# Optimization experiments

Measured on AMD Instinct MI355X. Metric: run time of the kernel, lower is better.

Reference implementation:

```python
import jax, jax.numpy as jnp
import numpy as np

DIM = 384
HEADS = 6
HEAD_DIM = DIM // HEADS
SCALE = HEAD_DIM ** -0.5


def setup_inputs() -> dict:
    key = jax.random.key(0)
    k1, k2, k3, k4, k5 = jax.random.split(key, 5)
    B, N, C = 2, 4096, DIM
    x = jax.random.normal(k1, (B, N, C), dtype=jnp.float32)
    mask = jax.random.randint(k2, (B, N), 0, 2) > 0  # bool [B, N]
    w_qkv = jax.random.normal(k3, (3 * C, C), dtype=jnp.float32) * (C ** -0.5)
    w_proj = jax.random.normal(k4, (C, C), dtype=jnp.float32) * (C ** -0.5)
    b_proj = jax.random.normal(k5, (C,), dtype=jnp.float32) * 0.01
    return {"x": x, "mask": mask, "w_qkv": w_qkv, "w_proj": w_proj, "b_proj": b_proj}


def reference(x, mask, w_qkv, w_proj, b_proj):
    B, N, C = x.shape
    # qkv projection (no bias), split into q, k, v of shape [B, H, N, hd]
    qkv = (x @ w_qkv.T).reshape(B, N, 3, HEADS, HEAD_DIM).transpose(2, 0, 3, 1, 4)
    q, k, v = qkv[0], qkv[1], qkv[2]
    attn = jnp.einsum('bhqd,bhkd->bhqk', q, k) * SCALE  # [B, H, N, N]
    # pairwise mask: mask[:, None, :] * mask[:, :, None], broadcast over heads
    pair = (mask[:, None, :, None] & mask[:, None, None, :])  # [B, 1, N, N]
    neg = -jnp.finfo(attn.dtype).max
    attn = jnp.where(pair, attn, neg)
    attn = jax.nn.softmax(attn, axis=-1)
    out = jnp.einsum('bhqk,bhkd->bhqd', attn, v)  # [B, H, N, hd]
    out = out.transpose(0, 2, 1, 3).reshape(B, N, C)
    return out @ w_proj.T + b_proj
```

## Files before the change

kernel.cpp:

```cpp
#include <hip/hip_runtime.h>
#include <cfloat>
#include <cstdint>
#include <cstddef>

using u16 = unsigned short;
typedef __attribute__((ext_vector_type(8))) short short8;
typedef __attribute__((ext_vector_type(4))) float f32x4;

#define HEADS 6
#define NSEQ 4096
#define SCALEF 0.125f
#define LOG2E 1.4426950408889634f
#define SC2 (SCALEF * LOG2E)

#if __has_builtin(__builtin_amdgcn_exp2f)
#define EXP2(x) __builtin_amdgcn_exp2f(x)
#else
#define EXP2(x) exp2f(x)
#endif

__device__ __forceinline__ u16 f2bf_rn(float f) {
  unsigned int u = __builtin_bit_cast(unsigned int, f);
  u = (u + 0x7FFFu + ((u >> 16) & 1u)) >> 16;
  return (u16)u;
}

__device__ __forceinline__ void gload_lds16(const void* g, void* l) {
  __builtin_amdgcn_global_load_lds((const __attribute__((address_space(1))) void*)g,
                                   (__attribute__((address_space(3))) void*)l, 16, 0, 0);
}

__device__ __forceinline__ short8 frag_read(const u16* tile, int row, int blk) {
  int byt = row * 128 + ((blk * 16) ^ ((row & 7) << 4));
  return *(const short8*)((const char*)tile + byt);
}

__device__ __forceinline__ void cast8(const float* __restrict__ s, u16* __restrict__ d, int i) {
  const float4* sp = (const float4*)s;
  float4 a = sp[2 * i], b = sp[2 * i + 1];
  short8 r;
  r[0] = (short)f2bf_rn(a.x); r[1] = (short)f2bf_rn(a.y);
  r[2] = (short)f2bf_rn(a.z); r[3] = (short)f2bf_rn(a.w);
  r[4] = (short)f2bf_rn(b.x); r[5] = (short)f2bf_rn(b.y);
  r[6] = (short)f2bf_rn(b.z); r[7] = (short)f2bf_rn(b.w);
  ((short8*)d)[i] = r;
}

__global__ void prep_kernel(const float* __restrict__ x, const float* __restrict__ wqkv,
                            const float* __restrict__ wproj, const int* __restrict__ mask,
                            u16* __restrict__ xb, u16* __restrict__ wqb, u16* __restrict__ wpb,
                            float* __restrict__ madd) {
  const int NX = 3145728 / 8, NQ = 442368 / 8, NP = 147456 / 8;
  int i = blockIdx.x * blockDim.x + threadIdx.x;
  if (i < NX) cast8(x, xb, i);
  else if (i < NX + NQ) cast8(wqkv, wqb, i - NX);
  else if (i < NX + NQ + NP) cast8(wproj, wpb, i - NX - NQ);
  else {
    int j = i - (NX + NQ + NP);
    if (j < 2 * NSEQ) madd[j] = mask[j] ? 0.f : -FLT_MAX;
  }
}

__global__ void compact_kernel(const int* __restrict__ mask, int* __restrict__ cpos,
                               float* __restrict__ acm, int* __restrict__ nth) {
  __shared__ int cnt[256];
  __shared__ int offu[256];
  __shared__ int s_nc;
  int b = blockIdx.x;
  int t = threadIdx.x;
  const int* m = mask + b * NSEQ;
  int base = t * 16;
  int c = 0;
#pragma unroll
  for (int i = 0; i < 16; ++i) c += (m[base + i] != 0) ? 1 : 0;
  cnt[t] = c;
  __syncthreads();
  if (t == 0) {
    int s = 0;
    for (int i = 0; i < 256; ++i) { offu[i] = s; s += cnt[i]; }
    s_nc = s;
    int ncpad = (s + 127) & ~127;
    if (ncpad == 0) ncpad = 128;
    nth[b] = ncpad / 128;
  }
  __syncthreads();
  int nc = s_nc;
  int ou = offu[t];
  int om = base - ou;
  for (int i = 0; i < 16; ++i) {
    int n = base + i;
    int um = (m[n] != 0) ? 1 : 0;
    int pos = um ? ou : (nc + om);
    ou += um;
    om += 1 - um;
    cpos[b * NSEQ + n] = pos;
    acm[b * NSEQ + pos] = um ? 0.f : -FLT_MAX;
  }
}

__global__ void meanv_kernel(const u16* __restrict__ vt, float* __restrict__ meanv) {
  int row = blockIdx.x;
  const u16* src = vt + (size_t)row * NSEQ + threadIdx.x * 8;
  float s = 0.f;
#pragma unroll
  for (int i = 0; i < 8; ++i) {
    short8 v = *(const short8*)(src + i * 512);
#pragma unroll
    for (int j = 0; j < 8; ++j) {
      unsigned int u = ((unsigned int)(unsigned short)v[j]) << 16;
      s += __builtin_bit_cast(float, u);
    }
  }
#pragma unroll
  for (int off = 1; off < 64; off <<= 1) s += __shfl_xor(s, off);
  if (threadIdx.x == 0) meanv[row] = s * (1.0f / NSEQ);
}

template <int EPI>
__launch_bounds__(256)
__global__ void gemm_bt(const u16* __restrict__ A, const u16* __restrict__ B,
                        int Kdim, int Ndim,
                        u16* __restrict__ q_out, u16* __restrict__ k_out, u16* __restrict__ vt_out,
                        const int* __restrict__ cpos,
                        const float* __restrict__ bias, float* __restrict__ out) {
  __shared__ u16 lA[128 * 64];
  __shared__ u16 lB[128 * 64];
  int brow = blockIdx.x, bcol = blockIdx.y;
  int tid = threadIdx.x;
  int w = tid >> 6, lane = tid & 63;
  int wr = w >> 1, wc = w & 1;
  int r_in = lane >> 3;
  int jblk = (lane & 7) ^ r_in;
  int l15 = lane & 15, lg = lane >> 4;

  f32x4 acc[4][4];
#pragma unroll
  for (int i = 0; i < 4; i++)
#pragma unroll
    for (int j = 0; j < 4; j++) acc[i][j] = (f32x4){0.f, 0.f, 0.f, 0.f};

  const u16* Ab = A + (size_t)(brow * 128 + w * 32 + r_in) * Kdim + jblk * 8;
  const u16* Bb = B + (size_t)(bcol * 128 + w * 32 + r_in) * Kdim + jblk * 8;

  int ksteps = Kdim >> 6;
  for (int kt = 0; kt < ksteps; ++kt) {
    __syncthreads();
#pragma unroll
    for (int c = 0; c < 4; ++c) {
      gload_lds16(Ab + kt * 64 + (size_t)(c * 8) * Kdim, &lA[(w * 32 + c * 8) * 64]);
      gload_lds16(Bb + kt * 64 + (size_t)(c * 8) * Kdim, &lB[(w * 32 + c * 8) * 64]);
    }
    asm volatile("s_waitcnt vmcnt(0)" ::: "memory");
    __syncthreads();

    short8 af[4][2], bfr[4][2];
#pragma unroll
    for (int ms = 0; ms < 4; ++ms)
#pragma unroll
      for (int hf = 0; hf < 2; ++hf)
        af[ms][hf] = frag_read(lA, wr * 64 + ms * 16 + l15, hf * 4 + lg);
#pragma unroll
    for (int ns = 0; ns < 4; ++ns)
#pragma unroll
      for (int hf = 0; hf < 2; ++hf)
        bfr[ns][hf] = frag_read(lB, wc * 64 + ns * 16 + l15, hf * 4 + lg);
#pragma unroll
    for (int ms = 0; ms < 4; ++ms)
#pragma unroll
      for (int ns = 0; ns < 4; ++ns) {
        acc[ms][ns] = __builtin_amdgcn_mfma_f32_16x16x32_bf16(af[ms][0], bfr[ns][0], acc[ms][ns], 0, 0, 0);
        acc[ms][ns] = __builtin_amdgcn_mfma_f32_16x16x32_bf16(af[ms][1], bfr[ns][1], acc[ms][ns], 0, 0, 0);
      }
  }

#pragma unroll
  for (int ms = 0; ms < 4; ++ms)
#pragma unroll
    for (int ns = 0; ns < 4; ++ns)
#pragma unroll
      for (int r = 0; r < 4; ++r) {
        int row_g = brow * 128 + wr * 64 + ms * 16 + lg * 4 + r;
        int col_g = bcol * 128 + wc * 64 + ns * 16 + l15;
        float v = acc[ms][ns][r];
        if (EPI == 0) {
          int t = col_g / 384;
          int rem = col_g - t * 384;
          int h = rem >> 6, d = rem & 63;
          int b = row_g >> 12, n = row_g & 4095;
          u16 val = f2bf_rn(v);
          size_t bh = (size_t)(b * HEADS + h);
          if (t == 0) {
            q_out[(bh * NSEQ + n) * 64 + d] = val;
          } else {
            int pp = cpos[row_g];
            if (t == 1) k_out[(bh * NSEQ + pp) * 64 + d] = val;
            else        vt_out[(bh * 64 + d) * NSEQ + pp] = val;
          }
        } else {
          out[(size_t)row_g * Ndim + col_g] = v + bias[col_g];
        }
      }
}

template <int KS>
__launch_bounds__(256, 3)
__global__ void attn_kernel32(const u16* __restrict__ qg, const u16* __restrict__ kg,
                              const u16* __restrict__ vtg, const float* __restrict__ madd,
                              const float* __restrict__ acm, const int* __restrict__ nth,
                              float* __restrict__ o_part, float* __restrict__ l_part) {
  __shared__ u16 lK[2][64 * 64];
  __shared__ u16 lV[2][64 * 64];

  int bid = blockIdx.x;
  int orig = (bid & 7) * (48 * KS) + (bid >> 3);
  int qb = orig & 31;
  int rr = orig >> 5;
  int bh = rr % 12, kh = rr / 12;

  int b = bh / HEADS;
  const int NT = nth[b];
  int kbase = kh * NT * 64;

  int tid = threadIdx.x;
  int w = tid >> 6, lane = tid & 63;
  int l15 = lane & 15, lg = lane >> 4;
  int r_in = lane >> 3, jblk = (lane & 7) ^ r_in;

  const u16* Q = qg + (size_t)bh * NSEQ * 64;
  const u16* K = kg + (size_t)bh * NSEQ * 64;
  const u16* VT = vtg + (size_t)bh * 64 * NSEQ;
  const float* marow = madd + b * NSEQ;
  const float* acrow = acm + b * NSEQ;

  int q0 = qb * 128 + w * 32;
  int qrow0 = q0 + l15, qrow1 = q0 + 16 + l15;
  short8 qfA[2], qfB[2];
#pragma unroll
  for (int hf = 0; hf < 2; ++hf) {
    qfA[hf] = *(const short8*)(Q + (size_t)qrow0 * 64 + hf * 32 + lg * 8);
    qfB[hf] = *(const short8*)(Q + (size_t)qrow1 * 64 + hf * 32 + lg * 8);
  }

  float qsel0 = (marow[qrow0] == 0.0f) ? 1.0f : 0.0f;
  float qsel1 = (marow[qrow1] == 0.0f) ? 1.0f : 0.0f;
  float scq0 = SC2 * qsel0, scq1 = SC2 * qsel1;

  int swk = (l15 & 7) << 4;
  int offKA = l15 * 128 + ((lg * 16) ^ swk);
  int offKB = l15 * 128 + (((4 + lg) * 16) ^ swk);

  f32x4 acc0[4], acc1[4];
#pragma unroll
  for (int ds_ = 0; ds_ < 4; ++ds_) {
    acc0[ds_] = (f32x4){0.f, 0.f, 0.f, 0.f};
    acc1[ds_] = (f32x4){0.f, 0.f, 0.f, 0.f};
  }
  f32x4 lsum0 = (f32x4){0.f, 0.f, 0.f, 0.f};
  f32x4 lsum1 = (f32x4){0.f, 0.f, 0.f, 0.f};

#define STAGE(BUF, k0s)                                                                     \
  {                                                                                         \
    _Pragma("unroll")                                                                       \
    for (int c = 0; c < 2; ++c) {                                                           \
      int rowb = w * 16 + c * 8;                                                            \
      gload_lds16(K + (size_t)((k0s) + rowb + r_in) * 64 + jblk * 8, &lK[BUF][rowb * 64]);  \
      gload_lds16(VT + (size_t)(rowb + r_in) * NSEQ + (k0s) + jblk * 8, &lV[BUF][rowb * 64]);\
    }                                                                                       \
  }

  STAGE(0, kbase);
  asm volatile("s_waitcnt vmcnt(0)" ::: "memory");
  __syncthreads();

  int cur = 0;
  for (int t = 0; t < NT; ++t) {
    if (t + 1 < NT) STAGE(cur ^ 1, kbase + (t + 1) * 64);

    const char* kb = (const char*)lK[cur];
    const char* vb = (const char*)lV[cur];

    f32x4 p0[4], p1[4];
    __builtin_amdgcn_s_setprio(1);
#pragma unroll
    for (int cs = 0; cs < 4; ++cs) {
      short8 kf0 = *(const short8*)(kb + offKA + cs * 2048);
      short8 kf1 = *(const short8*)(kb + offKB + cs * 2048);
      f32x4 z0 = (f32x4){0.f, 0.f, 0.f, 0.f};
      f32x4 z1 = (f32x4){0.f, 0.f, 0.f, 0.f};
      z0 = __builtin_amdgcn_mfma_f32_16x16x32_bf16(kf0, qfA[0], z0, 0, 0, 0);
      z1 = __builtin_amdgcn_mfma_f32_16x16x32_bf16(kf0, qfB[0], z1, 0, 0, 0);
      p0[cs] = __builtin_amdgcn_mfma_f32_16x16x32_bf16(kf1, qfA[1], z0, 0, 0, 0);
      p1[cs] = __builtin_amdgcn_mfma_f32_16x16x32_bf16(kf1, qfB[1], z1, 0, 0, 0);
    }
    __builtin_amdgcn_s_setprio(0);

    int k0 = kbase + t * 64;
#pragma unroll
    for (int cs = 0; cs < 4; ++cs) {
      f32x4 mf = *(const f32x4*)(acrow + k0 + cs * 16 + lg * 4);
      f32x4 d0 = p0[cs] * scq0 + mf * qsel0;
      f32x4 d1 = p1[cs] * scq1 + mf * qsel1;
#pragma unroll
      for (int r = 0; r < 4; ++r) {
        p0[cs][r] = EXP2(d0[r]);
        p1[cs][r] = EXP2(d1[r]);
      }
    }
    lsum0 += (p0[0] + p0[1]) + (p0[2] + p0[3]);
    lsum1 += (p1[0] + p1[1]) + (p1[2] + p1[3]);

    short8 pfA[2], pfB[2];
    {
      uint32_t wd[4][2];
#pragma unroll
      for (int cs = 0; cs < 4; ++cs)
#pragma unroll
        for (int hh = 0; hh < 2; ++hh)
          asm("v_cvt_pk_bf16_f32 %0, %1, %2" : "=v"(wd[cs][hh]) : "v"(p0[cs][2 * hh]), "v"(p0[cs][2 * hh + 1]));
#pragma unroll
      for (int c = 0; c < 2; ++c) {
        union { uint32_t u[4]; short8 s8; } cv;
#pragma unroll
        for (int hh = 0; hh < 2; ++hh) {
          uint32_t A = wd[2 * c][hh], B = wd[2 * c + 1][hh];
          asm("v_permlane32_swap_b32 %0, %1" : "+v"(A), "+v"(B));
          asm("v_permlane16_swap_b32 %0, %1" : "+v"(A), "+v"(B));
          cv.u[hh] = A;
          cv.u[2 + hh] = B;
        }
        pfA[c] = cv.s8;
      }
    }
    {
      uint32_t wd[4][2];
#pragma unroll
      for (int cs = 0; cs < 4; ++cs)
#pragma unroll
        for (int hh = 0; hh < 2; ++hh)
          asm("v_cvt_pk_bf16_f32 %0, %1, %2" : "=v"(wd[cs][hh]) : "v"(p1[cs][2 * hh]), "v"(p1[cs][2 * hh + 1]));
#pragma unroll
      for (int c = 0; c < 2; ++c) {
        union { uint32_t u[4]; short8 s8; } cv;
#pragma unroll
        for (int hh = 0; hh < 2; ++hh) {
          uint32_t A = wd[2 * c][hh], B = wd[2 * c + 1][hh];
          asm("v_permlane32_swap_b32 %0, %1" : "+v"(A), "+v"(B));
          asm("v_permlane16_swap_b32 %0, %1" : "+v"(A), "+v"(B));
          cv.u[hh] = A;
          cv.u[2 + hh] = B;
        }
        pfB[c] = cv.s8;
      }
    }

    __builtin_amdgcn_s_setprio(1);
#pragma unroll
    for (int ds_ = 0; ds_ < 4; ++ds_) {
      short8 vf0 = *(const short8*)(vb + offKA + ds_ * 2048);
      short8 vf1 = *(const short8*)(vb + offKB + ds_ * 2048);
      acc0[ds_] = __builtin_amdgcn_mfma_f32_16x16x32_bf16(vf0, pfA[0], acc0[ds_], 0, 0, 0);
      acc0[ds_] = __builtin_amdgcn_mfma_f32_16x16x32_bf16(vf1, pfA[1], acc0[ds_], 0, 0, 0);
      acc1[ds_] = __builtin_amdgcn_mfma_f32_16x16x32_bf16(vf0, pfB[0], acc1[ds_], 0, 0, 0);
      acc1[ds_] = __builtin_amdgcn_mfma_f32_16x16x32_bf16(vf1, pfB[1], acc1[ds_], 0, 0, 0);
    }
    __builtin_amdgcn_s_setprio(0);

    __syncthreads();
    cur ^= 1;
  }

  float rsum0 = (lsum0[0] + lsum0[1]) + (lsum0[2] + lsum0[3]);
  rsum0 += __shfl_xor(rsum0, 16);
  rsum0 += __shfl_xor(rsum0, 32);
  float rsum1 = (lsum1[0] + lsum1[1]) + (lsum1[2] + lsum1[3]);
  rsum1 += __shfl_xor(rsum1, 16);
  rsum1 += __shfl_xor(rsum1, 32);

  float* op = o_part + (size_t)kh * (8192ull * 384);
  int hd = bh - b * HEADS;
  size_t base0 = ((size_t)b * NSEQ + qrow0) * 384 + hd * 64;
  size_t base1 = ((size_t)b * NSEQ + qrow1) * 384 + hd * 64;
#pragma unroll
  for (int ds_ = 0; ds_ < 4; ++ds_) {
    *(f32x4*)(op + base0 + ds_ * 16 + lg * 4) = acc0[ds_];
    *(f32x4*)(op + base1 + ds_ * 16 + lg * 4) = acc1[ds_];
  }
  if (lg == 0) {
    l_part[(kh * 12 + bh) * NSEQ + qrow0] = rsum0;
    l_part[(kh * 12 + bh) * NSEQ + qrow1] = rsum1;
  }
#undef STAGE
}

template <int KS>
__global__ void combine_kernel(const float* __restrict__ o_part, const float* __restrict__ l_part,
                               const float* __restrict__ madd, const float* __restrict__ meanv,
                               u16* __restrict__ out) {
  int i = blockIdx.x * blockDim.x + threadIdx.x;
  int elem = i * 4;
  int ng = elem / 384;
  int cc = elem - ng * 384;
  int h = cc >> 6, d = cc & 63;
  int b = ng >> 12, n = ng & 4095;
  int li = (b * HEADS + h) * NSEQ + n;

  float4 a = ((const float4*)o_part)[i];
  float lt = l_part[li];
#pragma unroll
  for (int kh = 1; kh < KS; ++kh) {
    float4 c = ((const float4*)(o_part + (size_t)kh * (8192ull * 384)))[i];
    a.x += c.x; a.y += c.y; a.z += c.z; a.w += c.w;
    lt += l_part[kh * 12 * NSEQ + li];
  }
  float inv = 1.0f / lt;
  float a0 = a.x * inv, a1 = a.y * inv, a2 = a.z * inv, a3 = a.w * inv;
  if (madd[ng] != 0.0f) {
    const float* mv = meanv + (b * HEADS + h) * 64 + d;
    a0 = mv[0]; a1 = mv[1]; a2 = mv[2]; a3 = mv[3];
  }
  uint32_t w0, w1;
  asm("v_cvt_pk_bf16_f32 %0, %1, %2" : "=v"(w0) : "v"(a0), "v"(a1));
  asm("v_cvt_pk_bf16_f32 %0, %1, %2" : "=v"(w1) : "v"(a2), "v"(a3));
  uint2 st; st.x = w0; st.y = w1;
  *(uint2*)(out + elem) = st;
}

extern "C" void kernel_launch(void* const* d_in, const int* in_sizes, int n_in,
                              void* d_out, int out_size, void* d_ws, size_t ws_size,
                              hipStream_t stream) {
  const float* x = (const float*)d_in[0];
  const int* mask = (const int*)d_in[1];
  const float* w_qkv = (const float*)d_in[2];
  const float* w_proj = (const float*)d_in[3];
  const float* b_proj = (const float*)d_in[4];
  float* out = (float*)d_out;

  char* ws = (char*)d_ws;
  u16* x_bf = (u16*)(ws + 0);
  u16* wqkv_bf = (u16*)(ws + 6291456);
  u16* wproj_bf = (u16*)(ws + 7176192);
  u16* q_bf = (u16*)(ws + 7471104);
  u16* k_bf = (u16*)(ws + 13762560);
  u16* vt_bf = (u16*)(ws + 20054016);
  u16* attn_bf = (u16*)(ws + 26345472);
  float* madd = (float*)(ws + 32636928);
  float* o_part = (float*)(ws + 32669696);
  float* l_part = (float*)(ws + 57835520);
  int* cpos = (int*)(ws + 58228736);
  float* acm = (float*)(ws + 58261504);
  int* nth = (int*)(ws + 58294272);
  float* meanv = (float*)(ws + 58294288);

  const int NPREP = 3145728 / 8 + 442368 / 8 + 147456 / 8 + 2 * NSEQ;
  prep_kernel<<<(NPREP + 255) / 256, 256, 0, stream>>>(x, w_qkv, w_proj, mask,
                                                       x_bf, wqkv_bf, wproj_bf, madd);
  compact_kernel<<<2, 256, 0, stream>>>(mask, cpos, acm, nth);

  gemm_bt<0><<<dim3(64, 9), 256, 0, stream>>>(x_bf, wqkv_bf, 384, 1152,
                                              q_bf, k_bf, vt_bf, cpos, nullptr, nullptr);

  meanv_kernel<<<768, 64, 0, stream>>>(vt_bf, meanv);

  attn_kernel32<2><<<768, 256, 0, stream>>>(q_bf, k_bf, vt_bf, madd, acm, nth,
                                            o_part, l_part);
  combine_kernel<2><<<3072, 256, 0, stream>>>(o_part, l_part, madd, meanv, attn_bf);

  gemm_bt<1><<<dim3(64, 3), 256, 0, stream>>>(attn_bf, wproj_bf, 384, 384,
                                              nullptr, nullptr, nullptr, nullptr, b_proj, out);
}
```

Before: 109.2 us.

## Compact queries by mask, skip masked query tiles, split keys four ways

After: 93.09 us. 1.17x faster.

```diff
diff --git a/kernel.cpp b/kernel.cpp
--- a/kernel.cpp
+++ b/kernel.cpp
@@ -49,8 +49,46 @@
 __global__ void prep_kernel(const float* __restrict__ x, const float* __restrict__ wqkv,
                             const float* __restrict__ wproj, const int* __restrict__ mask,
                             u16* __restrict__ xb, u16* __restrict__ wqb, u16* __restrict__ wpb,
-                            float* __restrict__ madd) {
+                            float* __restrict__ madd,
+                            int* __restrict__ cpos, float* __restrict__ acm, int* __restrict__ nth) {
+  __shared__ int cnt[256];
+  __shared__ int offu[256];
+  __shared__ int s_nc;
   const int NX = 3145728 / 8, NQ = 442368 / 8, NP = 147456 / 8;
+  const int NPREP_BLK = 1856;
+  if (blockIdx.x >= NPREP_BLK) {
+    int b = blockIdx.x - NPREP_BLK;
+    int t = threadIdx.x;
+    const int* m = mask + b * NSEQ;
+    int base = t * 16;
+    int c = 0;
+#pragma unroll
+    for (int i = 0; i < 16; ++i) c += (m[base + i] != 0) ? 1 : 0;
+    cnt[t] = c;
+    __syncthreads();
+    if (t == 0) {
+      int s = 0;
+      for (int i = 0; i < 256; ++i) { offu[i] = s; s += cnt[i]; }
+      s_nc = s;
+      int ncpad = (s + 127) & ~127;
+      if (ncpad == 0) ncpad = 128;
+      nth[b] = ncpad / 128;
+    }
+    __syncthreads();
+    int nc = s_nc;
+    int ou = offu[t];
+    int om = base - ou;
+    for (int i = 0; i < 16; ++i) {
+      int n = base + i;
+      int um = (m[n] != 0) ? 1 : 0;
+      int pos = um ? ou : (nc + om);
+      ou += um;
+      om += 1 - um;
+      cpos[b * NSEQ + n] = pos;
+      acm[b * NSEQ + pos] = um ? 0.f : -FLT_MAX;
+    }
+    return;
+  }
   int i = blockIdx.x * blockDim.x + threadIdx.x;
   if (i < NX) cast8(x, xb, i);
   else if (i < NX + NQ) cast8(wqkv, wqb, i - NX);
@@ -58,43 +96,6 @@
   else {
     int j = i - (NX + NQ + NP);
     if (j < 2 * NSEQ) madd[j] = mask[j] ? 0.f : -FLT_MAX;
-  }
-}
-
-__global__ void compact_kernel(const int* __restrict__ mask, int* __restrict__ cpos,
-                               float* __restrict__ acm, int* __restrict__ nth) {
-  __shared__ int cnt[256];
-  __shared__ int offu[256];
-  __shared__ int s_nc;
-  int b = blockIdx.x;
-  int t = threadIdx.x;
-  const int* m = mask + b * NSEQ;
-  int base = t * 16;
-  int c = 0;
-#pragma unroll
-  for (int i = 0; i < 16; ++i) c += (m[base + i] != 0) ? 1 : 0;
-  cnt[t] = c;
-  __syncthreads();
-  if (t == 0) {
-    int s = 0;
-    for (int i = 0; i < 256; ++i) { offu[i] = s; s += cnt[i]; }
-    s_nc = s;
-    int ncpad = (s + 127) & ~127;
-    if (ncpad == 0) ncpad = 128;
-    nth[b] = ncpad / 128;
-  }
-  __syncthreads();
-  int nc = s_nc;
-  int ou = offu[t];
-  int om = base - ou;
-  for (int i = 0; i < 16; ++i) {
-    int n = base + i;
-    int um = (m[n] != 0) ? 1 : 0;
-    int pos = um ? ou : (nc + om);
-    ou += um;
-    om += 1 - um;
-    cpos[b * NSEQ + n] = pos;
-    acm[b * NSEQ + pos] = um ? 0.f : -FLT_MAX;
   }
 }
 
@@ -186,16 +187,13 @@
           int t = col_g / 384;
           int rem = col_g - t * 384;
           int h = rem >> 6, d = rem & 63;
-          int b = row_g >> 12, n = row_g & 4095;
+          int b = row_g >> 12;
           u16 val = f2bf_rn(v);
           size_t bh = (size_t)(b * HEADS + h);
-          if (t == 0) {
-            q_out[(bh * NSEQ + n) * 64 + d] = val;
-          } else {
-            int pp = cpos[row_g];
-            if (t == 1) k_out[(bh * NSEQ + pp) * 64 + d] = val;
-            else        vt_out[(bh * 64 + d) * NSEQ + pp] = val;
-          }
+          int pp = cpos[row_g];
+          if (t == 0)      q_out[(bh * NSEQ + pp) * 64 + d] = val;
+          else if (t == 1) k_out[(bh * NSEQ + pp) * 64 + d] = val;
+          else             vt_out[(bh * 64 + d) * NSEQ + pp] = val;
         } else {
           out[(size_t)row_g * Ndim + col_g] = v + bias[col_g];
         }
@@ -205,7 +203,7 @@
 template <int KS>
 __launch_bounds__(256, 3)
 __global__ void attn_kernel32(const u16* __restrict__ qg, const u16* __restrict__ kg,
-                              const u16* __restrict__ vtg, const float* __restrict__ madd,
+                              const u16* __restrict__ vtg,
                               const float* __restrict__ acm, const int* __restrict__ nth,
                               float* __restrict__ o_part, float* __restrict__ l_part) {
   __shared__ u16 lK[2][64 * 64];
@@ -218,8 +216,12 @@
   int bh = rr % 12, kh = rr / 12;
 
   int b = bh / HEADS;
-  const int NT = nth[b];
-  int kbase = kh * NT * 64;
+  const int nt_b = nth[b];
+  if (qb >= nt_b) return;
+  int kt_total = nt_b * 2;
+  int st = (kh * kt_total) / KS;
+  int NTL = ((kh + 1) * kt_total) / KS - st;
+  int kbase = st * 64;
 
   int tid = threadIdx.x;
   int w = tid >> 6, lane = tid & 63;
@@ -229,7 +231,6 @@
   const u16* Q = qg + (size_t)bh * NSEQ * 64;
   const u16* K = kg + (size_t)bh * NSEQ * 64;
   const u16* VT = vtg + (size_t)bh * 64 * NSEQ;
-  const float* marow = madd + b * NSEQ;
   const float* acrow = acm + b * NSEQ;
 
   int q0 = qb * 128 + w * 32;
@@ -241,8 +242,8 @@
     qfB[hf] = *(const short8*)(Q + (size_t)qrow1 * 64 + hf * 32 + lg * 8);
   }
 
-  float qsel0 = (marow[qrow0] == 0.0f) ? 1.0f : 0.0f;
-  float qsel1 = (marow[qrow1] == 0.0f) ? 1.0f : 0.0f;
+  float qsel0 = (acrow[qrow0] == 0.0f) ? 1.0f : 0.0f;
+  float qsel1 = (acrow[qrow1] == 0.0f) ? 1.0f : 0.0f;
   float scq0 = SC2 * qsel0, scq1 = SC2 * qsel1;
 
   int swk = (l15 & 7) << 4;
@@ -268,105 +269,107 @@
     }                                                                                       \
   }
 
-  STAGE(0, kbase);
-  asm volatile("s_waitcnt vmcnt(0)" ::: "memory");
-  __syncthreads();
-
-  int cur = 0;
-  for (int t = 0; t < NT; ++t) {
-    if (t + 1 < NT) STAGE(cur ^ 1, kbase + (t + 1) * 64);
-
-    const char* kb = (const char*)lK[cur];
-    const char* vb = (const char*)lV[cur];
-
-    f32x4 p0[4], p1[4];
-    __builtin_amdgcn_s_setprio(1);
-#pragma unroll
-    for (int cs = 0; cs < 4; ++cs) {
-      short8 kf0 = *(const short8*)(kb + offKA + cs * 2048);
-      short8 kf1 = *(const short8*)(kb + offKB + cs * 2048);
-      f32x4 z0 = (f32x4){0.f, 0.f, 0.f, 0.f};
-      f32x4 z1 = (f32x4){0.f, 0.f, 0.f, 0.f};
-      z0 = __builtin_amdgcn_mfma_f32_16x16x32_bf16(kf0, qfA[0], z0, 0, 0, 0);
-      z1 = __builtin_amdgcn_mfma_f32_16x16x32_bf16(kf0, qfB[0], z1, 0, 0, 0);
-      p0[cs] = __builtin_amdgcn_mfma_f32_16x16x32_bf16(kf1, qfA[1], z0, 0, 0, 0);
-      p1[cs] = __builtin_amdgcn_mfma_f32_16x16x32_bf16(kf1, qfB[1], z1, 0, 0, 0);
-    }
-    __builtin_amdgcn_s_setprio(0);
-
-    int k0 = kbase + t * 64;
-#pragma unroll
-    for (int cs = 0; cs < 4; ++cs) {
-      f32x4 mf = *(const f32x4*)(acrow + k0 + cs * 16 + lg * 4);
-      f32x4 d0 = p0[cs] * scq0 + mf * qsel0;
-      f32x4 d1 = p1[cs] * scq1 + mf * qsel1;
-#pragma unroll
-      for (int r = 0; r < 4; ++r) {
-        p0[cs][r] = EXP2(d0[r]);
-        p1[cs][r] = EXP2(d1[r]);
-      }
-    }
-    lsum0 += (p0[0] + p0[1]) + (p0[2] + p0[3]);
-    lsum1 += (p1[0] + p1[1]) + (p1[2] + p1[3]);
-
-    short8 pfA[2], pfB[2];
-    {
-      uint32_t wd[4][2];
-#pragma unroll
-      for (int cs = 0; cs < 4; ++cs)
-#pragma unroll
-        for (int hh = 0; hh < 2; ++hh)
-          asm("v_cvt_pk_bf16_f32 %0, %1, %2" : "=v"(wd[cs][hh]) : "v"(p0[cs][2 * hh]), "v"(p0[cs][2 * hh + 1]));
-#pragma unroll
-      for (int c = 0; c < 2; ++c) {
-        union { uint32_t u[4]; short8 s8; } cv;
-#pragma unroll
-        for (int hh = 0; hh < 2; ++hh) {
-          uint32_t A = wd[2 * c][hh], B = wd[2 * c + 1][hh];
-          asm("v_permlane32_swap_b32 %0, %1" : "+v"(A), "+v"(B));
-          asm("v_permlane16_swap_b32 %0, %1" : "+v"(A), "+v"(B));
-          cv.u[hh] = A;
-          cv.u[2 + hh] = B;
+  if (NTL > 0) {
+    STAGE(0, kbase);
+    asm volatile("s_waitcnt vmcnt(0)" ::: "memory");
+    __syncthreads();
+
+    int cur = 0;
+    for (int t = 0; t < NTL; ++t) {
+      if (t + 1 < NTL) STAGE(cur ^ 1, kbase + (t + 1) * 64);
+
+      const char* kb = (const char*)lK[cur];
+      const char* vb = (const char*)lV[cur];
+
+      f32x4 p0[4], p1[4];
+      __builtin_amdgcn_s_setprio(1);
+#pragma unroll
+      for (int cs = 0; cs < 4; ++cs) {
+        short8 kf0 = *(const short8*)(kb + offKA + cs * 2048);
+        short8 kf1 = *(const short8*)(kb + offKB + cs * 2048);
+        f32x4 z0 = (f32x4){0.f, 0.f, 0.f, 0.f};
+        f32x4 z1 = (f32x4){0.f, 0.f, 0.f, 0.f};
+        z0 = __builtin_amdgcn_mfma_f32_16x16x32_bf16(kf0, qfA[0], z0, 0, 0, 0);
+        z1 = __builtin_amdgcn_mfma_f32_16x16x32_bf16(kf0, qfB[0], z1, 0, 0, 0);
+        p0[cs] = __builtin_amdgcn_mfma_f32_16x16x32_bf16(kf1, qfA[1], z0, 0, 0, 0);
+        p1[cs] = __builtin_amdgcn_mfma_f32_16x16x32_bf16(kf1, qfB[1], z1, 0, 0, 0);
+      }
+      __builtin_amdgcn_s_setprio(0);
+
+      int k0 = kbase + t * 64;
+#pragma unroll
+      for (int cs = 0; cs < 4; ++cs) {
+        f32x4 mf = *(const f32x4*)(acrow + k0 + cs * 16 + lg * 4);
+        f32x4 d0 = p0[cs] * scq0 + mf * qsel0;
+        f32x4 d1 = p1[cs] * scq1 + mf * qsel1;
+#pragma unroll
+        for (int r = 0; r < 4; ++r) {
+          p0[cs][r] = EXP2(d0[r]);
+          p1[cs][r] = EXP2(d1[r]);
         }
-        pfA[c] = cv.s8;
-      }
-    }
-    {
-      uint32_t wd[4][2];
-#pragma unroll
-      for (int cs = 0; cs < 4; ++cs)
-#pragma unroll
-        for (int hh = 0; hh < 2; ++hh)
-          asm("v_cvt_pk_bf16_f32 %0, %1, %2" : "=v"(wd[cs][hh]) : "v"(p1[cs][2 * hh]), "v"(p1[cs][2 * hh + 1]));
-#pragma unroll
-      for (int c = 0; c < 2; ++c) {
-        union { uint32_t u[4]; short8 s8; } cv;
-#pragma unroll
-        for (int hh = 0; hh < 2; ++hh) {
-          uint32_t A = wd[2 * c][hh], B = wd[2 * c + 1][hh];
-          asm("v_permlane32_swap_b32 %0, %1" : "+v"(A), "+v"(B));
-          asm("v_permlane16_swap_b32 %0, %1" : "+v"(A), "+v"(B));
-          cv.u[hh] = A;
-          cv.u[2 + hh] = B;
+      }
+      lsum0 += (p0[0] + p0[1]) + (p0[2] + p0[3]);
+      lsum1 += (p1[0] + p1[1]) + (p1[2] + p1[3]);
+
+      short8 pfA[2], pfB[2];
+      {
+        uint32_t wd[4][2];
+#pragma unroll
+        for (int cs = 0; cs < 4; ++cs)
+#pragma unroll
+          for (int hh = 0; hh < 2; ++hh)
+            asm("v_cvt_pk_bf16_f32 %0, %1, %2" : "=v"(wd[cs][hh]) : "v"(p0[cs][2 * hh]), "v"(p0[cs][2 * hh + 1]));
+#pragma unroll
+        for (int c = 0; c < 2; ++c) {
+          union { uint32_t u[4]; short8 s8; } cv;
+#pragma unroll
+          for (int hh = 0; hh < 2; ++hh) {
+            uint32_t A = wd[2 * c][hh], B = wd[2 * c + 1][hh];
+            asm("v_permlane32_swap_b32 %0, %1" : "+v"(A), "+v"(B));
+            asm("v_permlane16_swap_b32 %0, %1" : "+v"(A), "+v"(B));
+            cv.u[hh] = A;
+            cv.u[2 + hh] = B;
+          }
+          pfA[c] = cv.s8;
         }
-        pfB[c] = cv.s8;
-      }
-    }
-
-    __builtin_amdgcn_s_setprio(1);
-#pragma unroll
-    for (int ds_ = 0; ds_ < 4; ++ds_) {
-      short8 vf0 = *(const short8*)(vb + offKA + ds_ * 2048);
-      short8 vf1 = *(const short8*)(vb + offKB + ds_ * 2048);
-      acc0[ds_] = __builtin_amdgcn_mfma_f32_16x16x32_bf16(vf0, pfA[0], acc0[ds_], 0, 0, 0);
-      acc0[ds_] = __builtin_amdgcn_mfma_f32_16x16x32_bf16(vf1, pfA[1], acc0[ds_], 0, 0, 0);
-      acc1[ds_] = __builtin_amdgcn_mfma_f32_16x16x32_bf16(vf0, pfB[0], acc1[ds_], 0, 0, 0);
-      acc1[ds_] = __builtin_amdgcn_mfma_f32_16x16x32_bf16(vf1, pfB[1], acc1[ds_], 0, 0, 0);
-    }
-    __builtin_amdgcn_s_setprio(0);
-
-    __syncthreads();
-    cur ^= 1;
+      }
+      {
+        uint32_t wd[4][2];
+#pragma unroll
+        for (int cs = 0; cs < 4; ++cs)
+#pragma unroll
+          for (int hh = 0; hh < 2; ++hh)
+            asm("v_cvt_pk_bf16_f32 %0, %1, %2" : "=v"(wd[cs][hh]) : "v"(p1[cs][2 * hh]), "v"(p1[cs][2 * hh + 1]));
+#pragma unroll
+        for (int c = 0; c < 2; ++c) {
+          union { uint32_t u[4]; short8 s8; } cv;
+#pragma unroll
+          for (int hh = 0; hh < 2; ++hh) {
+            uint32_t A = wd[2 * c][hh], B = wd[2 * c + 1][hh];
+            asm("v_permlane32_swap_b32 %0, %1" : "+v"(A), "+v"(B));
+            asm("v_permlane16_swap_b32 %0, %1" : "+v"(A), "+v"(B));
+            cv.u[hh] = A;
+            cv.u[2 + hh] = B;
+          }
+          pfB[c] = cv.s8;
+        }
+      }
+
+      __builtin_amdgcn_s_setprio(1);
+#pragma unroll
+      for (int ds_ = 0; ds_ < 4; ++ds_) {
+        short8 vf0 = *(const short8*)(vb + offKA + ds_ * 2048);
+        short8 vf1 = *(const short8*)(vb + offKB + ds_ * 2048);
+        acc0[ds_] = __builtin_amdgcn_mfma_f32_16x16x32_bf16(vf0, pfA[0], acc0[ds_], 0, 0, 0);
+        acc0[ds_] = __builtin_amdgcn_mfma_f32_16x16x32_bf16(vf1, pfA[1], acc0[ds_], 0, 0, 0);
+        acc1[ds_] = __builtin_amdgcn_mfma_f32_16x16x32_bf16(vf0, pfB[0], acc1[ds_], 0, 0, 0);
+        acc1[ds_] = __builtin_amdgcn_mfma_f32_16x16x32_bf16(vf1, pfB[1], acc1[ds_], 0, 0, 0);
+      }
+      __builtin_amdgcn_s_setprio(0);
+
+      __syncthreads();
+      cur ^= 1;
+    }
   }
 
   float rsum0 = (lsum0[0] + lsum0[1]) + (lsum0[2] + lsum0[3]);
@@ -395,28 +398,32 @@
 template <int KS>
 __global__ void combine_kernel(const float* __restrict__ o_part, const float* __restrict__ l_part,
                                const float* __restrict__ madd, const float* __restrict__ meanv,
-                               u16* __restrict__ out) {
+                               const int* __restrict__ cpos, u16* __restrict__ out) {
   int i = blockIdx.x * blockDim.x + threadIdx.x;
   int elem = i * 4;
   int ng = elem / 384;
   int cc = elem - ng * 384;
   int h = cc >> 6, d = cc & 63;
-  int b = ng >> 12, n = ng & 4095;
-  int li = (b * HEADS + h) * NSEQ + n;
-
-  float4 a = ((const float4*)o_part)[i];
-  float lt = l_part[li];
-#pragma unroll
-  for (int kh = 1; kh < KS; ++kh) {
-    float4 c = ((const float4*)(o_part + (size_t)kh * (8192ull * 384)))[i];
-    a.x += c.x; a.y += c.y; a.z += c.z; a.w += c.w;
-    lt += l_part[kh * 12 * NSEQ + li];
-  }
-  float inv = 1.0f / lt;
-  float a0 = a.x * inv, a1 = a.y * inv, a2 = a.z * inv, a3 = a.w * inv;
+  int b = ng >> 12;
+
+  float a0, a1, a2, a3;
   if (madd[ng] != 0.0f) {
     const float* mv = meanv + (b * HEADS + h) * 64 + d;
     a0 = mv[0]; a1 = mv[1]; a2 = mv[2]; a3 = mv[3];
+  } else {
+    int pos = cpos[ng];
+    size_t pbase = (size_t)(b * NSEQ + pos) * 384 + cc;
+    int li = (b * HEADS + h) * NSEQ + pos;
+    float4 a = *(const float4*)(o_part + pbase);
+    float lt = l_part[li];
+#pragma unroll
+    for (int kh = 1; kh < KS; ++kh) {
+      float4 c = *(const float4*)(o_part + (size_t)kh * (8192ull * 384) + pbase);
+      a.x += c.x; a.y += c.y; a.z += c.z; a.w += c.w;
+      lt += l_part[kh * 12 * NSEQ + li];
+    }
+    float inv = 1.0f / lt;
+    a0 = a.x * inv; a1 = a.y * inv; a2 = a.z * inv; a3 = a.w * inv;
   }
   uint32_t w0, w1;
   asm("v_cvt_pk_bf16_f32 %0, %1, %2" : "=v"(w0) : "v"(a0), "v"(a1));
@@ -444,26 +451,31 @@
   u16* vt_bf = (u16*)(ws + 20054016);
   u16* attn_bf = (u16*)(ws + 26345472);
   float* madd = (float*)(ws + 32636928);
-  float* o_part = (float*)(ws + 32669696);
-  float* l_part = (float*)(ws + 57835520);
-  int* cpos = (int*)(ws + 58228736);
-  float* acm = (float*)(ws + 58261504);
-  int* nth = (int*)(ws + 58294272);
-  float* meanv = (float*)(ws + 58294288);
-
-  const int NPREP = 3145728 / 8 + 442368 / 8 + 147456 / 8 + 2 * NSEQ;
-  prep_kernel<<<(NPREP + 255) / 256, 256, 0, stream>>>(x, w_qkv, w_proj, mask,
-                                                       x_bf, wqkv_bf, wproj_bf, madd);
-  compact_kernel<<<2, 256, 0, stream>>>(mask, cpos, acm, nth);
+  int* cpos = (int*)(ws + 32669696);
+  float* acm = (float*)(ws + 32702464);
+  int* nth = (int*)(ws + 32735232);
+  float* meanv = (float*)(ws + 32735296);
+  float* o_part = (float*)(ws + 32738432);
+
+  const int NPREP_GRID = 1856 + 2;
+  prep_kernel<<<NPREP_GRID, 256, 0, stream>>>(x, w_qkv, w_proj, mask,
+                                              x_bf, wqkv_bf, wproj_bf, madd,
+                                              cpos, acm, nth);
 
   gemm_bt<0><<<dim3(64, 9), 256, 0, stream>>>(x_bf, wqkv_bf, 384, 1152,
                                               q_bf, k_bf, vt_bf, cpos, nullptr, nullptr);
 
   meanv_kernel<<<768, 64, 0, stream>>>(vt_bf, meanv);
 
-  attn_kernel32<2><<<768, 256, 0, stream>>>(q_bf, k_bf, vt_bf, madd, acm, nth,
-                                            o_part, l_part);
-  combine_kernel<2><<<3072, 256, 0, stream>>>(o_part, l_part, madd, meanv, attn_bf);
+  if (ws_size >= 32738432ull + 4ull * 12582912 + 4ull * 196608) {
+    float* l_part = (float*)(ws + 32738432 + 4ull * 12582912);
+    attn_kernel32<4><<<1536, 256, 0, stream>>>(q_bf, k_bf, vt_bf, acm, nth, o_part, l_part);
+    combine_kernel<4><<<3072, 256, 0, stream>>>(o_part, l_part, madd, meanv, cpos, attn_bf);
+  } else {
+    float* l_part = (float*)(ws + 32738432 + 2ull * 12582912);
+    attn_kernel32<2><<<768, 256, 0, stream>>>(q_bf, k_bf, vt_bf, acm, nth, o_part, l_part);
+    combine_kernel<2><<<3072, 256, 0, stream>>>(o_part, l_part, madd, meanv, cpos, attn_bf);
+  }
 
   gemm_bt<1><<<dim3(64, 3), 256, 0, stream>>>(attn_bf, wproj_bf, 384, 384,
                                               nullptr, nullptr, nullptr, nullptr, b_proj, out);
```
